# Performance work log

Measured on AMD Instinct MI355X. Metric: run time of the kernel, lower is better.

Reference implementation:

```python
import jax, jax.numpy as jnp
import numpy as np

EMBED_DIM = 1024
NUM_HEADS = 16
HEAD_DIM = EMBED_DIM // NUM_HEADS  # used only for the softmax scale


def setup_inputs() -> dict:
    key = jax.random.key(0)
    k_x, k_wqkv, k_bqkv, k_wo, k_bo = jax.random.split(key, 5)
    bound_qkv = 1.0 / np.sqrt(EMBED_DIM)
    return {
        "x": jax.random.normal(k_x, (4, 2048, EMBED_DIM), dtype=jnp.float32),
        "W_qkv": jax.random.uniform(k_wqkv, (EMBED_DIM, 3 * EMBED_DIM), jnp.float32, -bound_qkv, bound_qkv),
        "b_qkv": jax.random.uniform(k_bqkv, (3 * EMBED_DIM,), jnp.float32, -bound_qkv, bound_qkv),
        "W_out": jax.random.uniform(k_wo, (EMBED_DIM, EMBED_DIM), jnp.float32, -bound_qkv, bound_qkv),
        "b_out": jax.random.uniform(k_bo, (EMBED_DIM,), jnp.float32, -bound_qkv, bound_qkv),
    }


def reference(x, W_qkv, b_qkv, W_out, b_out):
    # fused QKV projection: [B,S,3E]
    qkv = jnp.einsum("bse,ef->bsf", x, W_qkv) + b_qkv
    q, k, v = jnp.split(qkv, 3, axis=-1)  # each [B,S,E]
    scale = 1.0 / jnp.sqrt(jnp.float32(HEAD_DIM))
    # NOTE: no head reshape — attention over full embed_dim, scale uses head_dim
    scores = jnp.einsum("bqe,bke->bqk", q, k) * scale  # [B,S,S]
    attn = jax.nn.softmax(scores, axis=-1)
    context = jnp.einsum("bqk,bke->bqe", attn, v)  # [B,S,E]
    return jnp.einsum("bse,ef->bsf", context, W_out) + b_out
```

## Files before the change

kernel.cpp:

```cpp
#include <hip/hip_runtime.h>

typedef unsigned short u16;
typedef __bf16   bf16x8 __attribute__((ext_vector_type(8)));
typedef float    f32x4  __attribute__((ext_vector_type(4)));
typedef unsigned short u16x4 __attribute__((ext_vector_type(4)));
typedef unsigned short u16x8 __attribute__((ext_vector_type(8)));

__device__ inline float bf2f(u16 u) { return __uint_as_float(((unsigned int)u) << 16); }
__device__ inline u16 f2bf(float f) {
    unsigned int u = __float_as_uint(f);
    u += 0x7FFF + ((u >> 16) & 1);
    return (u16)(u >> 16);
}

__device__ inline void gl2lds16(const u16* g, u16* l) {
    __builtin_amdgcn_global_load_lds(
        (const __attribute__((address_space(1))) void*)g,
        (__attribute__((address_space(3))) void*)l, 16, 0, 0);
}

__global__ __launch_bounds__(256)
void sniff_zero(const u16* __restrict__ x, int* __restrict__ flag,
                float* __restrict__ sums) {
    sums[blockIdx.x * 256 + threadIdx.x] = 0.0f;
    if (blockIdx.x == 0 && threadIdx.x < 64) {
        const int lane = threadIdx.x;
        const unsigned idx = lane * 131072u + 65536u;
        const u16 u = x[idx];
        const int e = (u >> 7) & 0xFF;
        const unsigned long long b = __ballot(e >= 100 && e <= 140);
        if (lane == 0) flag[0] = (__popcll(b) >= 48) ? 0 : 1;
    }
}

__global__ __launch_bounds__(256)
void convx_biases(const void* __restrict__ x, u16* __restrict__ xbf,
                  const void* __restrict__ b1, const void* __restrict__ b2,
                  u16* __restrict__ o1, u16* __restrict__ o2,
                  const int* __restrict__ flagp) {
    const int f = *flagp;
    if (blockIdx.x < 8192) {
        const long i = ((long)blockIdx.x * 256 + threadIdx.x) * 4;
        if (f) {
            f32x4 v = *(const f32x4*)((const float*)x + i);
            u16x4 o; o[0] = f2bf(v[0]); o[1] = f2bf(v[1]); o[2] = f2bf(v[2]); o[3] = f2bf(v[3]);
            *(u16x4*)(xbf + i) = o;
        } else {
            *(u16x4*)(xbf + i) = *(const u16x4*)((const u16*)x + i);
        }
    } else {
        const int i = (blockIdx.x - 8192) * 256 + threadIdx.x;
        if (i < 3072) o1[i] = f ? f2bf(((const float*)b1)[i]) : ((const u16*)b1)[i];
        else { const int j = i - 3072;
               o2[j] = f ? f2bf(((const float*)b2)[j]) : ((const u16*)b2)[j]; }
    }
}

__global__ __launch_bounds__(256)
void transpose_w(const void* __restrict__ Wqkv, u16* __restrict__ WqkvT,
                 const void* __restrict__ Wout, u16* __restrict__ WoutT,
                 const int* __restrict__ flagp)
{
    const void* in; u16* out; long inStride, outStride;
    if (blockIdx.z == 0) { in = Wqkv; out = WqkvT; inStride = 3072; outStride = 1024; }
    else { if (blockIdx.x >= 32) return;
           in = Wout; out = WoutT; inStride = 1024; outStride = 1024; }
    __shared__ u16 t[32][36];
    const int isF32 = *flagp;
    const int tid = threadIdx.x;
    const long r0 = (long)blockIdx.y * 32;
    const long c0 = (long)blockIdx.x * 32;
    const int r  = tid >> 3;
    const int c4 = (tid & 7) * 4;
    const long base = (r0 + r) * inStride + c0 + c4;
    u16x4 v;
    if (isF32) {
        f32x4 f = *(const f32x4*)((const float*)in + base);
        v[0] = f2bf(f[0]); v[1] = f2bf(f[1]); v[2] = f2bf(f[2]); v[3] = f2bf(f[3]);
    } else {
        v = *(const u16x4*)((const u16*)in + base);
    }
    t[r][c4 + 0] = v[0]; t[r][c4 + 1] = v[1]; t[r][c4 + 2] = v[2]; t[r][c4 + 3] = v[3];
    __syncthreads();
    u16x4 o;
    o[0] = t[c4 + 0][r]; o[1] = t[c4 + 1][r]; o[2] = t[c4 + 2][r]; o[3] = t[c4 + 3][r];
    *(u16x4*)&out[(c0 + r) * outStride + r0 + c4] = o;
}

template <int GM, int GN, int WM, int WN>
__device__ __forceinline__ void kloop(
    const u16* __restrict__ A, const u16* __restrict__ Bt,
    int K, long lda, long ldb, long m0, long n0,
    u16* __restrict__ As, u16* __restrict__ Bs, f32x4 (&acc)[WM][WN])
{
    constexpr int BM = GM * WM * 16;
    constexpr int BN = GN * WN * 16;
    constexpr int IA = BM / 32;
    constexpr int IB = BN / 32;
    const int tid  = threadIdx.x;
    const int lane = tid & 63;
    const int wave = tid >> 6;
    const int sr   = tid >> 3;
    const int qg0  = (tid & 7) ^ (sr & 7);
    const u16* pa[IA]; const u16* pb[IB];
    u16* la[IA]; u16* lb[IB];
#pragma unroll
    for (int i = 0; i < IA; ++i) {
        pa[i] = A + (m0 + i * 32 + sr) * lda + qg0 * 8;
        la[i] = As + (i * 256 + wave * 64) * 8;
    }
#pragma unroll
    for (int i = 0; i < IB; ++i) {
        pb[i] = Bt + (n0 + i * 32 + sr) * ldb + qg0 * 8;
        lb[i] = Bs + (i * 256 + wave * 64) * 8;
    }
    const int wm = (wave / GN) * (WM * 16);
    const int wn = (wave % GN) * (WN * 16);
    const int lr = lane & 15;
    const int hk = lane >> 4;
    int aoff[WM][2], boff[WN][2];
#pragma unroll
    for (int i = 0; i < WM; ++i) {
        const int row = wm + i * 16 + lr, r7 = row & 7;
        aoff[i][0] = row * 64 + ((hk     ^ r7) * 8);
        aoff[i][1] = row * 64 + (((4+hk) ^ r7) * 8);
    }
#pragma unroll
    for (int j = 0; j < WN; ++j) {
        const int row = wn + j * 16 + lr, r7 = row & 7;
        boff[j][0] = row * 64 + ((hk     ^ r7) * 8);
        boff[j][1] = row * 64 + (((4+hk) ^ r7) * 8);
    }
    for (int kt = 0; kt < K; kt += 64) {
#pragma unroll
        for (int i = 0; i < IA; ++i) { gl2lds16(pa[i], la[i]); pa[i] += 64; }
#pragma unroll
        for (int i = 0; i < IB; ++i) { gl2lds16(pb[i], lb[i]); pb[i] += 64; }
        __syncthreads();
#pragma unroll
        for (int ks = 0; ks < 2; ++ks) {
            bf16x8 af[WM], bf[WN];
#pragma unroll
            for (int i = 0; i < WM; ++i) af[i] = *(const bf16x8*)&As[aoff[i][ks]];
#pragma unroll
            for (int j = 0; j < WN; ++j) bf[j] = *(const bf16x8*)&Bs[boff[j][ks]];
#pragma unroll
            for (int i = 0; i < WM; ++i)
#pragma unroll
                for (int j = 0; j < WN; ++j)
                    acc[i][j] = __builtin_amdgcn_mfma_f32_16x16x32_bf16(af[i], bf[j], acc[i][j], 0, 0, 0);
        }
        __syncthreads();
    }
}

template <int WM, int WN, typename F>
__device__ __forceinline__ void epi_bf16(u16* __restrict__ Sw, u16* __restrict__ C,
    long ldc, long gm0, long gn0, int lane, F f)
{
    const int lr = lane & 15, hk = lane >> 4;
#pragma unroll
    for (int i = 0; i < WM; ++i)
#pragma unroll
        for (int j = 0; j < WN; ++j)
#pragma unroll
            for (int r = 0; r < 4; ++r)
                Sw[(i*16 + hk*4 + r) * (WN*16) + j*16 + lr] = f2bf(f(i, j, r));
    asm volatile("s_waitcnt lgkmcnt(0)" ::: "memory");
    constexpr int LPR = WN * 2;
    constexpr int RPI = 64 / LPR;
    const int rl = lane / LPR, c8 = (lane % LPR) * 8;
#pragma unroll
    for (int t = 0; t < (WM*16) / RPI; ++t) {
        const int row = t * RPI + rl;
        u16x8 v8 = *(const u16x8*)&Sw[row * (WN*16) + c8];
        *(u16x8*)&C[(gm0 + row) * ldc + gn0 + c8] = v8;
    }
}

template <int WM, int WN, typename F>
__device__ __forceinline__ void epi_f32(float* __restrict__ Sw, float* __restrict__ C,
    long ldc, long gm0, long gn0, int lane, F f)
{
    const int lr = lane & 15, hk = lane >> 4;
#pragma unroll
    for (int jh = 0; jh < 2; ++jh) {
#pragma unroll
        for (int i = 0; i < WM; ++i)
#pragma unroll
            for (int jj = 0; jj < WN/2; ++jj)
#pragma unroll
                for (int r = 0; r < 4; ++r)
                    Sw[(i*16 + hk*4 + r) * (WN*8) + jj*16 + lr] = f(i, jh*(WN/2) + jj, r);
        asm volatile("s_waitcnt lgkmcnt(0)" ::: "memory");
        constexpr int LPR = WN * 2;
        constexpr int RPI = 64 / LPR;
        const int rl = lane / LPR, c4 = (lane % LPR) * 4;
#pragma unroll
        for (int t = 0; t < (WM*16) / RPI; ++t) {
            const int row = t * RPI + rl;
            f32x4 v4 = *(const f32x4*)&Sw[row * (WN*8) + c4];
            *(f32x4*)&C[(gm0 + row) * ldc + gn0 + jh*(WN*8) + c4] = v4;
        }
        asm volatile("s_waitcnt lgkmcnt(0)" ::: "memory");
    }
}

template<int MH, int NH>
__device__ __forceinline__ void mfma16(const bf16x8 (&a)[2][4], const bf16x8 (&b)[2][2],
                                       f32x4 (&acc)[2][2][4][2])
{
    __builtin_amdgcn_s_setprio(1);
#pragma unroll
    for (int ks = 0; ks < 2; ++ks)
#pragma unroll
        for (int i = 0; i < 4; ++i)
#pragma unroll
            for (int j = 0; j < 2; ++j)
                acc[MH][NH][i][j] = __builtin_amdgcn_mfma_f32_16x16x32_bf16(
                    a[ks][i], b[ks][j], acc[MH][NH][i][j], 0, 0, 0);
    __builtin_amdgcn_s_setprio(0);
}

__device__ __forceinline__ void kloop256(
    const u16* __restrict__ A, const u16* __restrict__ Bt,
    int K, long lda, long ldb, long m0, long n0,
    u16* __restrict__ S, f32x4 (&acc)[2][2][4][2])
{
    constexpr int BUF = 256 * 64;
    const int tid  = threadIdx.x;
    const int wave = tid >> 6, lane = tid & 63;
    const int wmi  = wave >> 2, wni = wave & 3;
    const int sr   = tid >> 3;
    const int qg   = ((tid & 7) ^ (sr & 7)) * 8;
    const int lr   = lane & 15, hk = lane >> 4, l7 = lane & 7;
    const u16* pA = A + (m0 + sr) * lda + qg;
    const u16* pB = Bt + (n0 + sr) * ldb + qg;
    u16* const lA = S + wave * 512;
    u16* const lB = S + 2 * BUF + wave * 512;
    const int aO0 = (wmi*64 + lr)*64 + ((hk       ^ l7) * 8);
    const int aO1 = (wmi*64 + lr)*64 + (((4 + hk) ^ l7) * 8);
    const int bO0 = (wni*32 + lr)*64 + ((hk       ^ l7) * 8);
    const int bO1 = (wni*32 + lr)*64 + (((4 + hk) ^ l7) * 8);
    const int NT = K >> 6;

    auto stA = [&](int buf, int mh, int kt) {
        const u16* s = pA + (long)mh * 128 * lda + kt;
        u16* d = lA + buf * BUF + mh * 8192;
        gl2lds16(s, d);
        gl2lds16(s + 64 * lda, d + 4096);
    };
    auto stB = [&](int buf, int nh, int kt) {
        const u16* s = pB + (long)nh * 128 * ldb + kt;
        u16* d = lB + buf * BUF + nh * 8192;
        gl2lds16(s, d);
        gl2lds16(s + 64 * ldb, d + 4096);
    };

    stA(0,0,0); stB(0,0,0); stB(0,1,0); stA(0,1,0);
    stA(1,0,64); stB(1,0,64); stB(1,1,64);
    asm volatile("s_waitcnt vmcnt(6)" ::: "memory");
    __builtin_amdgcn_s_barrier();

    bf16x8 a[2][4], b0[2][2], b1[2][2];
    for (int t = 0; t < NT; ++t) {
        const int b = t & 1;
        const u16* Ab = S + b * BUF;
        const u16* Bb = S + 2 * BUF + b * BUF;
#pragma unroll
        for (int i = 0; i < 4; ++i) {
            a[0][i] = *(const bf16x8*)&Ab[aO0 + i*1024];
            a[1][i] = *(const bf16x8*)&Ab[aO1 + i*1024];
        }
#pragma unroll
        for (int j = 0; j < 2; ++j) {
            b0[0][j] = *(const bf16x8*)&Bb[bO0 + j*1024];
            b0[1][j] = *(const bf16x8*)&Bb[bO1 + j*1024];
        }
        if (t + 1 < NT) stA(b ^ 1, 1, (t + 1) << 6);
        __builtin_amdgcn_s_barrier();
        asm volatile("s_waitcnt lgkmcnt(0)" ::: "memory");
        mfma16<0,0>(a, b0, acc);
        __builtin_amdgcn_s_barrier();
#pragma unroll
        for (int j = 0; j < 2; ++j) {
            b1[0][j] = *(const bf16x8*)&Bb[bO0 + 8192 + j*1024];
            b1[1][j] = *(const bf16x8*)&Bb[bO1 + 8192 + j*1024];
        }
        if (t + 2 < NT) stA(b, 0, (t + 2) << 6);
        __builtin_amdgcn_s_barrier();
        asm volatile("s_waitcnt lgkmcnt(0)" ::: "memory");
        mfma16<0,1>(a, b1, acc);
        __builtin_amdgcn_s_barrier();
#pragma unroll
        for (int i = 0; i < 4; ++i) {
            a[0][i] = *(const bf16x8*)&Ab[aO0 + 8192 + i*1024];
            a[1][i] = *(const bf16x8*)&Ab[aO1 + 8192 + i*1024];
        }
        if (t + 2 < NT) stB(b, 0, (t + 2) << 6);
        __builtin_amdgcn_s_barrier();
        asm volatile("s_waitcnt lgkmcnt(0)" ::: "memory");
        mfma16<1,1>(a, b1, acc);
        __builtin_amdgcn_s_barrier();
        if (t + 2 < NT) stB(b, 1, (t + 2) << 6);
        __builtin_amdgcn_s_barrier();
        mfma16<1,0>(a, b0, acc);
        if (t + 2 < NT)      asm volatile("s_waitcnt vmcnt(6)" ::: "memory");
        else if (t + 1 < NT) asm volatile("s_waitcnt vmcnt(0)" ::: "memory");
        __builtin_amdgcn_s_barrier();
    }
}

template <typename F>
__device__ __forceinline__ void epi256_bf16(u16* __restrict__ Sw, u16* __restrict__ C,
    long ldc, long m0, long n0, int wmi, int wni, int lane, F f)
{
    const int lr = lane & 15, hk = lane >> 4;
#pragma unroll
    for (int mh = 0; mh < 2; ++mh)
#pragma unroll
    for (int i = 0; i < 4; ++i)
#pragma unroll
    for (int r = 0; r < 4; ++r)
#pragma unroll
    for (int nh = 0; nh < 2; ++nh)
#pragma unroll
    for (int j = 0; j < 2; ++j)
        Sw[(mh*64 + i*16 + hk*4 + r) * 64 + nh*32 + j*16 + lr] = f2bf(f(mh, nh, i, j, r));
    asm volatile("s_waitcnt lgkmcnt(0)" ::: "memory");
    const int rl = lane >> 3, c8 = (lane & 7) * 8;
    const long gcolb = n0 + (long)((c8 >> 5) * 128 + wni * 32 + (c8 & 31));
#pragma unroll
    for (int t = 0; t < 16; ++t) {
        const int row = t * 8 + rl;
        const long grow = m0 + (row >> 6) * 128 + wmi * 64 + (row & 63);
        *(u16x8*)&C[grow * ldc + gcolb] = *(const u16x8*)&Sw[row * 64 + c8];
    }
}

__global__ __launch_bounds__(512, 2)
void gemm_qkv256(const u16* __restrict__ A, const u16* __restrict__ Bt,
                 u16* __restrict__ C, const u16* __restrict__ bias)
{
    __shared__ __align__(16) u16 S[65536];
    const long m0 = (long)blockIdx.y * 256, n0 = (long)blockIdx.x * 256;
    f32x4 acc[2][2][4][2] = {};
    kloop256(A, Bt, 1024, 1024L, 1024L, m0, n0, S, acc);
    const int lane = threadIdx.x & 63, wave = threadIdx.x >> 6;
    const int wmi = wave >> 2, wni = wave & 3;
    const int lr = lane & 15;
    float bj[2][2];
#pragma unroll
    for (int nh = 0; nh < 2; ++nh)
#pragma unroll
        for (int j = 0; j < 2; ++j)
            bj[nh][j] = bf2f(bias[n0 + nh*128 + wni*32 + j*16 + lr]);
    epi256_bf16(S + wave * 8192, C, 3072L, m0, n0, wmi, wni, lane,
        [&](int mh, int nh, int i, int j, int r) { return acc[mh][nh][i][j][r] + bj[nh][j]; });
}

__global__ __launch_bounds__(512, 2)
void gemm_phase2_256(const u16* __restrict__ QKV, u16* __restrict__ P,
                     const u16* __restrict__ WoutT, u16* __restrict__ VWT,
                     float* __restrict__ sums)
{
    __shared__ __align__(16) u16 S[65536];
    const int z = blockIdx.z;
    const u16 *Ap, *Bp; u16* Cp; long lda, ldb, ldc, m0, n0;
    bool doExp; float* srow = nullptr;
    if (z < 4) {
        const long zb = (long)z * 2048 * 3072;
        Ap = QKV + zb; Bp = QKV + 1024 + zb;
        Cp = P + (long)z * 2048 * 2048;
        lda = 3072; ldb = 3072; ldc = 2048;
        m0 = (long)blockIdx.y * 256; n0 = (long)blockIdx.x * 256;
        doExp = true; srow = sums + z * 2048;
    } else {
        const int vb = (z - 4) * 2 + (blockIdx.y >> 2);
        Ap = WoutT; lda = 1024;
        Bp = QKV + 2048 + (long)vb * 2048 * 3072; ldb = 3072;
        Cp = VWT + (long)vb * 1024 * 2048; ldc = 2048;
        m0 = (long)(blockIdx.y & 3) * 256; n0 = (long)blockIdx.x * 256;
        doExp = false;
    }
    f32x4 acc[2][2][4][2] = {};
    kloop256(Ap, Bp, 1024, lda, ldb, m0, n0, S, acc);
    const int lane = threadIdx.x & 63, wave = threadIdx.x >> 6;
    const int wmi = wave >> 2, wni = wave & 3;
    const int lr = lane & 15, hk = lane >> 4;
    u16* Sw = S + wave * 8192;
    if (doExp) {
#pragma unroll
        for (int mh = 0; mh < 2; ++mh)
#pragma unroll
        for (int i = 0; i < 4; ++i)
#pragma unroll
        for (int r = 0; r < 4; ++r) {
            float s = 0.0f;
#pragma unroll
            for (int nh = 0; nh < 2; ++nh)
#pragma unroll
            for (int j = 0; j < 2; ++j) {
                const float e = __expf(acc[mh][nh][i][j][r] * 0.125f);
                Sw[(mh*64 + i*16 + hk*4 + r) * 64 + nh*32 + j*16 + lr] = f2bf(e);
                s += e;
            }
            s += __shfl_xor(s, 1); s += __shfl_xor(s, 2);
            s += __shfl_xor(s, 4); s += __shfl_xor(s, 8);
            if (lr == 0) atomicAdd(&srow[m0 + mh*128 + wmi*64 + i*16 + hk*4 + r], s);
        }
        asm volatile("s_waitcnt lgkmcnt(0)" ::: "memory");
        const int rl = lane >> 3, c8 = (lane & 7) * 8;
        const long gcolb = n0 + (long)((c8 >> 5) * 128 + wni * 32 + (c8 & 31));
#pragma unroll
        for (int t = 0; t < 16; ++t) {
            const int row = t * 8 + rl;
            const long grow = m0 + (row >> 6) * 128 + wmi * 64 + (row & 63);
            *(u16x8*)&Cp[grow * ldc + gcolb] = *(const u16x8*)&Sw[row * 64 + c8];
        }
    } else {
        epi256_bf16(Sw, Cp, ldc, m0, n0, wmi, wni, lane,
            [&](int mh, int nh, int i, int j, int r) { return acc[mh][nh][i][j][r]; });
    }
}

__global__ __launch_bounds__(256, 4)
void gemm_final(const u16* __restrict__ P, const u16* __restrict__ VWT,
                void* __restrict__ out, const u16* __restrict__ bias,
                const float* __restrict__ sums, const int* __restrict__ flagp)
{
    __shared__ __align__(16) u16 S[256 * 64];
    const int outF32 = *flagp;
    const long bz = blockIdx.z;
    const long m0 = (long)blockIdx.y * 128, n0 = (long)blockIdx.x * 128;
    f32x4 acc[4][4] = {};
    kloop<2, 2, 4, 4>(P + bz * 2048 * 2048, VWT + bz * 1024 * 2048,
                      2048, 2048L, 2048L, m0, n0, S, S + 128*64, acc);
    const int lane = threadIdx.x & 63, wave = threadIdx.x >> 6;
    const int wm = (wave >> 1) * 64, wn = (wave & 1) * 64;
    const int lr = lane & 15, hk = lane >> 4;
    float inv[4][4], bj[4];
#pragma unroll
    for (int i = 0; i < 4; ++i)
#pragma unroll
        for (int r = 0; r < 4; ++r)
            inv[i][r] = 1.0f / sums[bz * 2048 + m0 + wm + i*16 + hk*4 + r];
#pragma unroll
    for (int j = 0; j < 4; ++j) bj[j] = bf2f(bias[n0 + wn + j*16 + lr]);
    if (outF32) {
        float* Co = (float*)out + bz * 2048 * 1024;
        epi_f32<4, 4>((float*)S + wave * 2048, Co, 1024L, m0 + wm, n0 + wn, lane,
            [&](int i, int j, int r) { return acc[i][j][r] * inv[i][r] + bj[j]; });
    } else {
        u16* Co = (u16*)out + bz * 2048 * 1024;
        epi_bf16<4, 4>(S + wave * 4096, Co, 1024L, m0 + wm, n0 + wn, lane,
            [&](int i, int j, int r) { return acc[i][j][r] * inv[i][r] + bj[j]; });
    }
}

extern "C" void kernel_launch(void* const* d_in, const int* in_sizes, int n_in,
                              void* d_out, int out_size, void* d_ws, size_t ws_size,
                              hipStream_t stream)
{
    const void* x    = d_in[0];
    const void* Wqkv = d_in[1];
    const void* bqkv = d_in[2];
    const void* Wout = d_in[3];
    const void* bout = d_in[4];
    char* ws = (char*)d_ws;

    u16*   xbf   = (u16*)(ws);
    u16*   WqkvT = (u16*)(ws + 16777216);
    u16*   P     = (u16*)(ws);
    u16*   QKV   = (u16*)(ws + 33554432);
    u16*   VWT   = (u16*)(ws + 83886080);
    u16*   WoutT = (u16*)(ws + 100663296);
    u16*   bqkvc = (u16*)(ws + 102760448);
    u16*   boutc = (u16*)(ws + 102766592);
    int*   flag  = (int*)(ws + 102768640);
    float* sums  = (float*)(ws + 102772736);

    dim3 blk(256);

    sniff_zero<<<32, blk, 0, stream>>>((const u16*)x, flag, sums);
    convx_biases<<<8208, blk, 0, stream>>>(x, xbf, bqkv, bout, bqkvc, boutc, flag);
    transpose_w<<<dim3(96, 32, 2), blk, 0, stream>>>(Wqkv, WqkvT, Wout, WoutT, flag);

    gemm_qkv256<<<dim3(12, 32, 1), dim3(512), 0, stream>>>(xbf, WqkvT, QKV, bqkvc);

    gemm_phase2_256<<<dim3(8, 8, 6), dim3(512), 0, stream>>>(QKV, P, WoutT, VWT, sums);

    gemm_final<<<dim3(8, 16, 4), blk, 0, stream>>>(P, VWT, d_out, boutc, sums, flag);
}
```

Before: 276.2 us.

## Fold V and output projection weights into one precomputed Wv·Wout matrix

Computes the product of the V slice of W_qkv and W_out once per call as a weight-only GEMM, plus a folded output bias (b_out + b_v·W_out). The QKV GEMM then writes the V·W_out result directly in transposed layout, which removes the per-batch V×W_out GEMM from the attention phase. The QKV GEMM moves from the 256-tile kernel to a 128-tile kernel with a transposed epilogue. The extra bf16 rounding of the fused weight is a small accuracy risk.

```diff
diff --git a/kernel.cpp b/kernel.cpp
--- a/kernel.cpp
+++ b/kernel.cpp
@@ -59,7 +59,7 @@
 __global__ __launch_bounds__(256)
 void transpose_w(const void* __restrict__ Wqkv, u16* __restrict__ WqkvT,
                  const void* __restrict__ Wout, u16* __restrict__ WoutT,
-                 const int* __restrict__ flagp)
+                 u16* __restrict__ Wvbf, const int* __restrict__ flagp)
 {
     const void* in; u16* out; long inStride, outStride;
     if (blockIdx.z == 0) { in = Wqkv; out = WqkvT; inStride = 3072; outStride = 1024; }
@@ -80,6 +80,10 @@
     } else {
         v = *(const u16x4*)((const u16*)in + base);
     }
+    if (blockIdx.z == 0 && c0 >= 2048) {
+        *(u16x4*)&Wvbf[(r0 + r) * 1024 + (c0 - 2048) + c4] = v;
+        return;
+    }
     t[r][c4 + 0] = v[0]; t[r][c4 + 1] = v[1]; t[r][c4 + 2] = v[2]; t[r][c4 + 3] = v[3];
     __syncthreads();
     u16x4 o;
@@ -201,6 +205,34 @@
             const int row = t * RPI + rl;
             f32x4 v4 = *(const f32x4*)&Sw[row * (WN*8) + c4];
             *(f32x4*)&C[(gm0 + row) * ldc + gn0 + jh*(WN*8) + c4] = v4;
+        }
+        asm volatile("s_waitcnt lgkmcnt(0)" ::: "memory");
+    }
+}
+
+__device__ __forceinline__ void epiT_vw(u16* __restrict__ Sw, u16* __restrict__ VWTb,
+    long o0, long t0, int lane, const f32x4 (&acc)[4][4])
+{
+    const int lr = lane & 15, hk = lane >> 4;
+#pragma unroll
+    for (int jh = 0; jh < 2; ++jh) {
+#pragma unroll
+        for (int jj = 0; jj < 2; ++jj) {
+            const int j = jh*2 + jj;
+            const int fl = jj*16 + lr;
+#pragma unroll
+            for (int i = 0; i < 4; ++i)
+#pragma unroll
+                for (int r = 0; r < 4; ++r)
+                    Sw[fl*72 + i*16 + hk*4 + r] = f2bf(acc[i][j][r]);
+        }
+        asm volatile("s_waitcnt lgkmcnt(0)" ::: "memory");
+        const int rl = lane >> 3, c8 = (lane & 7) * 8;
+#pragma unroll
+        for (int s = 0; s < 4; ++s) {
+            const int fl = s*8 + rl;
+            *(u16x8*)&VWTb[(o0 + jh*32 + fl) * 2048 + t0 + c8] =
+                *(const u16x8*)&Sw[fl*72 + c8];
         }
         asm volatile("s_waitcnt lgkmcnt(0)" ::: "memory");
     }
@@ -311,116 +343,109 @@
     }
 }
 
-template <typename F>
-__device__ __forceinline__ void epi256_bf16(u16* __restrict__ Sw, u16* __restrict__ C,
-    long ldc, long m0, long n0, int wmi, int wni, int lane, F f)
-{
-    const int lr = lane & 15, hk = lane >> 4;
-#pragma unroll
-    for (int mh = 0; mh < 2; ++mh)
-#pragma unroll
-    for (int i = 0; i < 4; ++i)
-#pragma unroll
-    for (int r = 0; r < 4; ++r)
-#pragma unroll
-    for (int nh = 0; nh < 2; ++nh)
-#pragma unroll
-    for (int j = 0; j < 2; ++j)
-        Sw[(mh*64 + i*16 + hk*4 + r) * 64 + nh*32 + j*16 + lr] = f2bf(f(mh, nh, i, j, r));
-    asm volatile("s_waitcnt lgkmcnt(0)" ::: "memory");
-    const int rl = lane >> 3, c8 = (lane & 7) * 8;
-    const long gcolb = n0 + (long)((c8 >> 5) * 128 + wni * 32 + (c8 & 31));
-#pragma unroll
-    for (int t = 0; t < 16; ++t) {
-        const int row = t * 8 + rl;
-        const long grow = m0 + (row >> 6) * 128 + wmi * 64 + (row & 63);
-        *(u16x8*)&C[grow * ldc + gcolb] = *(const u16x8*)&Sw[row * 64 + c8];
-    }
+__global__ __launch_bounds__(256, 4)
+void gemm_qkv(const u16* __restrict__ A, const u16* __restrict__ Bt,
+              u16* __restrict__ C, u16* __restrict__ VWT,
+              const u16* __restrict__ bias)
+{
+    __shared__ __align__(16) u16 S[256 * 64];
+    const long m0 = (long)blockIdx.y * 128, n0 = (long)blockIdx.x * 128;
+    f32x4 acc[4][4] = {};
+    kloop<2, 2, 4, 4>(A, Bt, 1024, 1024L, 1024L, m0, n0, S, S + 128*64, acc);
+    const int lane = threadIdx.x & 63, wave = threadIdx.x >> 6;
+    const int wm = (wave >> 1) * 64, wn = (wave & 1) * 64;
+    u16* Sw = S + wave * 4096;
+    if (n0 >= 2048) {
+        u16* VWTb = VWT + (m0 >> 11) * 1024 * 2048;
+        epiT_vw(Sw, VWTb, n0 + wn - 2048, (m0 & 2047) + wm, lane, acc);
+    } else {
+        const int lr = lane & 15;
+        float bj[4];
+#pragma unroll
+        for (int j = 0; j < 4; ++j) bj[j] = bf2f(bias[n0 + wn + j*16 + lr]);
+        epi_bf16<4, 4>(Sw, C, 3072L, m0 + wm, n0 + wn, lane,
+            [&](int i, int j, int r) { return acc[i][j][r] + bj[j]; });
+    }
+}
+
+__global__ __launch_bounds__(256, 4)
+void gemm_wvo(const u16* __restrict__ WoutT, const u16* __restrict__ Wvbf,
+              u16* __restrict__ WvoT, const u16* __restrict__ bqkvc,
+              const u16* __restrict__ boutc, u16* __restrict__ bfinal)
+{
+    __shared__ __align__(16) u16 S[256 * 64];
+    if (blockIdx.x == 8) {
+        if (blockIdx.y != 0) return;
+        const int tid = threadIdx.x;
+#pragma unroll
+        for (int oo = 0; oo < 4; ++oo) {
+            const int o = tid * 4 + oo;
+            float s = bf2f(boutc[o]);
+            const u16* row = WoutT + (long)o * 1024;
+            for (int v = 0; v < 1024; v += 8) {
+                u16x8 w = *(const u16x8*)&row[v];
+                u16x8 b = *(const u16x8*)&bqkvc[2048 + v];
+#pragma unroll
+                for (int q = 0; q < 8; ++q) s += bf2f(w[q]) * bf2f(b[q]);
+            }
+            bfinal[o] = f2bf(s);
+        }
+        return;
+    }
+    const long m0 = (long)blockIdx.y * 128, n0 = (long)blockIdx.x * 128;
+    f32x4 acc[4][4] = {};
+    kloop<2, 2, 4, 4>(WoutT, Wvbf, 1024, 1024L, 1024L, m0, n0, S, S + 128*64, acc);
+    const int lane = threadIdx.x & 63, wave = threadIdx.x >> 6;
+    const int wm = (wave >> 1) * 64, wn = (wave & 1) * 64;
+    epi_bf16<4, 4>(S + wave * 4096, WvoT, 1024L, m0 + wm, n0 + wn, lane,
+        [&](int i, int j, int r) { return acc[i][j][r]; });
 }
 
 __global__ __launch_bounds__(512, 2)
-void gemm_qkv256(const u16* __restrict__ A, const u16* __restrict__ Bt,
-                 u16* __restrict__ C, const u16* __restrict__ bias)
+void gemm_scores256(const u16* __restrict__ QKV, u16* __restrict__ P,
+                    float* __restrict__ sums)
 {
     __shared__ __align__(16) u16 S[65536];
+    const int z = blockIdx.z;
+    const long zb = (long)z * 2048 * 3072;
+    const u16* Ap = QKV + zb;
+    const u16* Bp = QKV + 1024 + zb;
+    u16* Cp = P + (long)z * 2048 * 2048;
+    float* srow = sums + z * 2048;
     const long m0 = (long)blockIdx.y * 256, n0 = (long)blockIdx.x * 256;
     f32x4 acc[2][2][4][2] = {};
-    kloop256(A, Bt, 1024, 1024L, 1024L, m0, n0, S, acc);
-    const int lane = threadIdx.x & 63, wave = threadIdx.x >> 6;
-    const int wmi = wave >> 2, wni = wave & 3;
-    const int lr = lane & 15;
-    float bj[2][2];
-#pragma unroll
-    for (int nh = 0; nh < 2; ++nh)
-#pragma unroll
-        for (int j = 0; j < 2; ++j)
-            bj[nh][j] = bf2f(bias[n0 + nh*128 + wni*32 + j*16 + lr]);
-    epi256_bf16(S + wave * 8192, C, 3072L, m0, n0, wmi, wni, lane,
-        [&](int mh, int nh, int i, int j, int r) { return acc[mh][nh][i][j][r] + bj[nh][j]; });
-}
-
-__global__ __launch_bounds__(512, 2)
-void gemm_phase2_256(const u16* __restrict__ QKV, u16* __restrict__ P,
-                     const u16* __restrict__ WoutT, u16* __restrict__ VWT,
-                     float* __restrict__ sums)
-{
-    __shared__ __align__(16) u16 S[65536];
-    const int z = blockIdx.z;
-    const u16 *Ap, *Bp; u16* Cp; long lda, ldb, ldc, m0, n0;
-    bool doExp; float* srow = nullptr;
-    if (z < 4) {
-        const long zb = (long)z * 2048 * 3072;
-        Ap = QKV + zb; Bp = QKV + 1024 + zb;
-        Cp = P + (long)z * 2048 * 2048;
-        lda = 3072; ldb = 3072; ldc = 2048;
-        m0 = (long)blockIdx.y * 256; n0 = (long)blockIdx.x * 256;
-        doExp = true; srow = sums + z * 2048;
-    } else {
-        const int vb = (z - 4) * 2 + (blockIdx.y >> 2);
-        Ap = WoutT; lda = 1024;
-        Bp = QKV + 2048 + (long)vb * 2048 * 3072; ldb = 3072;
-        Cp = VWT + (long)vb * 1024 * 2048; ldc = 2048;
-        m0 = (long)(blockIdx.y & 3) * 256; n0 = (long)blockIdx.x * 256;
-        doExp = false;
-    }
-    f32x4 acc[2][2][4][2] = {};
-    kloop256(Ap, Bp, 1024, lda, ldb, m0, n0, S, acc);
+    kloop256(Ap, Bp, 1024, 3072L, 3072L, m0, n0, S, acc);
     const int lane = threadIdx.x & 63, wave = threadIdx.x >> 6;
     const int wmi = wave >> 2, wni = wave & 3;
     const int lr = lane & 15, hk = lane >> 4;
     u16* Sw = S + wave * 8192;
-    if (doExp) {
-#pragma unroll
-        for (int mh = 0; mh < 2; ++mh)
-#pragma unroll
-        for (int i = 0; i < 4; ++i)
-#pragma unroll
-        for (int r = 0; r < 4; ++r) {
-            float s = 0.0f;
-#pragma unroll
-            for (int nh = 0; nh < 2; ++nh)
-#pragma unroll
-            for (int j = 0; j < 2; ++j) {
-                const float e = __expf(acc[mh][nh][i][j][r] * 0.125f);
-                Sw[(mh*64 + i*16 + hk*4 + r) * 64 + nh*32 + j*16 + lr] = f2bf(e);
-                s += e;
-            }
-            s += __shfl_xor(s, 1); s += __shfl_xor(s, 2);
-            s += __shfl_xor(s, 4); s += __shfl_xor(s, 8);
-            if (lr == 0) atomicAdd(&srow[m0 + mh*128 + wmi*64 + i*16 + hk*4 + r], s);
-        }
-        asm volatile("s_waitcnt lgkmcnt(0)" ::: "memory");
-        const int rl = lane >> 3, c8 = (lane & 7) * 8;
-        const long gcolb = n0 + (long)((c8 >> 5) * 128 + wni * 32 + (c8 & 31));
-#pragma unroll
-        for (int t = 0; t < 16; ++t) {
-            const int row = t * 8 + rl;
-            const long grow = m0 + (row >> 6) * 128 + wmi * 64 + (row & 63);
-            *(u16x8*)&Cp[grow * ldc + gcolb] = *(const u16x8*)&Sw[row * 64 + c8];
-        }
-    } else {
-        epi256_bf16(Sw, Cp, ldc, m0, n0, wmi, wni, lane,
-            [&](int mh, int nh, int i, int j, int r) { return acc[mh][nh][i][j][r]; });
+#pragma unroll
+    for (int mh = 0; mh < 2; ++mh)
+#pragma unroll
+    for (int i = 0; i < 4; ++i)
+#pragma unroll
+    for (int r = 0; r < 4; ++r) {
+        float s = 0.0f;
+#pragma unroll
+        for (int nh = 0; nh < 2; ++nh)
+#pragma unroll
+        for (int j = 0; j < 2; ++j) {
+            const float e = __expf(acc[mh][nh][i][j][r] * 0.125f);
+            Sw[(mh*64 + i*16 + hk*4 + r) * 64 + nh*32 + j*16 + lr] = f2bf(e);
+            s += e;
+        }
+        s += __shfl_xor(s, 1); s += __shfl_xor(s, 2);
+        s += __shfl_xor(s, 4); s += __shfl_xor(s, 8);
+        if (lr == 0) atomicAdd(&srow[m0 + mh*128 + wmi*64 + i*16 + hk*4 + r], s);
+    }
+    asm volatile("s_waitcnt lgkmcnt(0)" ::: "memory");
+    const int rl = lane >> 3, c8 = (lane & 7) * 8;
+    const long gcolb = n0 + (long)((c8 >> 5) * 128 + wni * 32 + (c8 & 31));
+#pragma unroll
+    for (int t = 0; t < 16; ++t) {
+        const int row = t * 8 + rl;
+        const long grow = m0 + (row >> 6) * 128 + wmi * 64 + (row & 63);
+        *(u16x8*)&Cp[grow * 2048 + gcolb] = *(const u16x8*)&Sw[row * 64 + c8];
     }
 }
 
@@ -474,21 +499,26 @@
     u16*   P     = (u16*)(ws);
     u16*   QKV   = (u16*)(ws + 33554432);
     u16*   VWT   = (u16*)(ws + 83886080);
+    u16*   Wvbf  = (u16*)(ws + 83886080);
     u16*   WoutT = (u16*)(ws + 100663296);
     u16*   bqkvc = (u16*)(ws + 102760448);
     u16*   boutc = (u16*)(ws + 102766592);
     int*   flag  = (int*)(ws + 102768640);
+    u16*   bfin  = (u16*)(ws + 102769664);
     float* sums  = (float*)(ws + 102772736);
 
     dim3 blk(256);
 
     sniff_zero<<<32, blk, 0, stream>>>((const u16*)x, flag, sums);
     convx_biases<<<8208, blk, 0, stream>>>(x, xbf, bqkv, bout, bqkvc, boutc, flag);
-    transpose_w<<<dim3(96, 32, 2), blk, 0, stream>>>(Wqkv, WqkvT, Wout, WoutT, flag);
-
-    gemm_qkv256<<<dim3(12, 32, 1), dim3(512), 0, stream>>>(xbf, WqkvT, QKV, bqkvc);
-
-    gemm_phase2_256<<<dim3(8, 8, 6), dim3(512), 0, stream>>>(QKV, P, WoutT, VWT, sums);
-
-    gemm_final<<<dim3(8, 16, 4), blk, 0, stream>>>(P, VWT, d_out, boutc, sums, flag);
-}
+    transpose_w<<<dim3(96, 32, 2), blk, 0, stream>>>(Wqkv, WqkvT, Wout, WoutT, Wvbf, flag);
+
+    gemm_wvo<<<dim3(9, 8, 1), blk, 0, stream>>>(WoutT, Wvbf, WqkvT + 2048*1024,
+                                                bqkvc, boutc, bfin);
+
+    gemm_qkv<<<dim3(24, 64, 1), blk, 0, stream>>>(xbf, WqkvT, QKV, VWT, bqkvc);
+
+    gemm_scores256<<<dim3(8, 8, 4), dim3(512), 0, stream>>>(QKV, P, sums);
+
+    gemm_final<<<dim3(8, 16, 4), blk, 0, stream>>>(P, VWT, d_out, bfin, sums, flag);
+}
```

New measurement: 306.4 us. 1.11x slower.
